# Kernel optimization log

Measured on AMD Instinct MI355X. Metric: run time of the kernel, lower is better.

## Reference

```python
import jax, jax.numpy as jnp
import numpy as np

TAU = 0.05
BETA = 8.0
MAX_ITERS = 6
EPS = 1e-12  # torch F.normalize eps


def setup_inputs() -> dict:
    key = jax.random.key(0)
    P, d, C, h = 20000, 128, 512, 4
    k1, k2, k3, k4 = jax.random.split(key, 4)
    K = jax.random.normal(k1, (P, d), dtype=jnp.float32) * 0.1
    Theta = jax.random.normal(k2, (C, d, h), dtype=jnp.float32)
    head_idx = jax.random.randint(k3, (C,), 0, P)
    initial_val = jax.random.uniform(k4, (P,), dtype=jnp.float32)
    return {"K": K, "Theta": Theta, "head_idx": head_idx, "initial_val": initial_val}


def _l2norm(x, axis):
    n = jnp.sqrt(jnp.sum(x * x, axis=axis, keepdims=True))
    return x / jnp.maximum(n, EPS)


def reference(K, Theta, head_idx, initial_val):
    P = K.shape[0]
    C, d, h = Theta.shape
    Kn = _l2norm(K, axis=1)            # [P, d]
    Thetan = _l2norm(Theta, axis=1)    # [C, d, h] (normalize over d, per slot)
    # cosine similarity per clause/slot: S[c, p, s]
    S = jnp.einsum('pd,cds->cps', Kn, Thetan)          # [C, P, h]
    best = jnp.argmax(S, axis=1)                        # [C, h] best predicate per slot
    conf = jnp.take_along_axis(S, best[:, None, :], axis=1)[:, 0, :]  # [C, h]
    beta_eff = max(BETA, 1.0)
    n = 2 * h
    log_n = jnp.float32(np.log(n))

    val = initial_val
    for _ in range(MAX_ITERS):
        vals = val[best]                                # [C, h] truth values at argmax preds
        combined = jnp.concatenate([conf, vals], axis=1)  # [C, 2h]
        # softmin_tau(x) = -(1/tau) * (logsumexp(-x/tau) - log n)
        g = -(1.0 / TAU) * (jax.nn.logsumexp(-combined / TAU, axis=1) - log_n)
        g = jnp.clip(g, 0.0, 1.0)                       # [C]
        # soft OR per head: (1/beta) * logsumexp(beta * g) over clauses sharing a head
        e = jax.ops.segment_sum(jnp.exp(beta_eff * g), head_idx, num_segments=P)
        g_head = jnp.log(jnp.maximum(e, 1e-38)) / beta_eff
        val = jnp.where(e > 0, jnp.maximum(val, g_head), val)
    return val
```

## Files before the change

### kernel.cpp

```cpp
#include <hip/hip_runtime.h>
#include <hip/hip_bf16.h>
#include <math.h>

#define D_DIM 128
#define H_DIM 4
#define QCAP 1024

typedef __attribute__((ext_vector_type(4))) float f32x4;
typedef __attribute__((ext_vector_type(8))) __bf16 bf16x8v;

__device__ inline unsigned int f2bf(float f) {
    __hip_bfloat16 b = __float2bfloat16(f);
    return (unsigned int)*reinterpret_cast<unsigned short*>(&b);
}
__device__ inline unsigned int encf(float v) {
    unsigned int u = __float_as_uint(v);
    return (u & 0x80000000u) ? ~u : (u | 0x80000000u);
}
__device__ inline float decf(unsigned int ub) {
    unsigned int fb = (ub & 0x80000000u) ? (ub ^ 0x80000000u) : ~ub;
    return __uint_as_float(fb);
}

__global__ __launch_bounds__(256) void k_prep(
    const float* __restrict__ K, unsigned int* __restrict__ Knb,
    float* __restrict__ rnK,
    const float* __restrict__ Theta, unsigned int* __restrict__ Tnb,
    float* __restrict__ Tn32,
    const float* __restrict__ initial, float* __restrict__ out,
    int* __restrict__ head_of, int P, int Ppad, int NJ)
{
    int wave = threadIdx.x >> 6, lane = threadIdx.x & 63;
    int row = blockIdx.x * 4 + wave;
    if (row < Ppad) {
        if (row >= P) {
            Knb[(size_t)row * 64 + lane] = 0u;
        } else {
            float2 v = ((const float2*)(K + (size_t)row * D_DIM))[lane];
            float ss = v.x * v.x + v.y * v.y;
            #pragma unroll
            for (int off = 1; off < 64; off <<= 1) ss += __shfl_xor(ss, off);
            float rn = 1.0f / fmaxf(sqrtf(ss), 1e-12f);
            Knb[(size_t)row * 64 + lane] = f2bf(v.x * rn) | (f2bf(v.y * rn) << 16);
            if (lane == 0) {
                rnK[row] = rn;
                out[row] = initial[row];
                head_of[row] = 0x7FFFFFFF;
            }
        }
    }
    if (blockIdx.x < (NJ >> 2)) {
        int j = blockIdx.x * 4 + wave;
        int c = j >> 2, s = j & 3;
        const float* base = Theta + (size_t)c * (D_DIM * H_DIM) + s;
        float t0 = base[(2 * lane) * H_DIM];
        float t1 = base[(2 * lane + 1) * H_DIM];
        float ss = t0 * t0 + t1 * t1;
        #pragma unroll
        for (int off = 1; off < 64; off <<= 1) ss += __shfl_xor(ss, off);
        float rn = 1.0f / fmaxf(sqrtf(ss), 1e-12f);
        float n0 = t0 * rn, n1 = t1 * rn;
        Tnb[(size_t)j * 64 + lane] = f2bf(n0) | (f2bf(n1) << 16);
        float2 w2; w2.x = n0; w2.y = n1;
        ((float2*)(Tn32 + (size_t)j * D_DIM))[lane] = w2;
    }
}

__global__ __launch_bounds__(256) void k_fused3(
    const unsigned short* __restrict__ Knb, const unsigned short* __restrict__ Tnb,
    const float* __restrict__ K, const float* __restrict__ rnK,
    const float* __restrict__ Tn32,
    unsigned int* __restrict__ gmax, unsigned long long* __restrict__ cand,
    int P)
{
    __shared__ __align__(16) unsigned short As[128 * 128];
    __shared__ __align__(16) unsigned short Bs[128 * 128];
    __shared__ float sred[5 * 512];
    __shared__ float thrl[128];
    __shared__ unsigned short queue[QCAP];
    __shared__ int qn;

    const int tid = threadIdx.x;
    const int lane = tid & 63;
    const int wave = tid >> 6;
    if (tid == 0) qn = 0;

    const int jt = blockIdx.x >> 5;
    const int w  = blockIdx.x & 31;
    const int begin = (w < 29) ? w * 5 : 29 * 5 + (w - 29) * 4;
    const int cnt   = (w < 29) ? 5 : 4;
    const int j0 = jt * 128;

    const int rr = lane >> 4, cc = lane & 15;

    {
        const unsigned short* gA = Tnb + (size_t)j0 * 128;
        const unsigned short* gB = Knb + (size_t)(begin * 128) * 128;
        #pragma unroll
        for (int i = 0; i < 8; i++) {
            int r0 = wave * 32 + i * 4;
            int rw = r0 + rr;
            int sc = (cc ^ (rw & 7)) << 3;
            __builtin_amdgcn_global_load_lds(
                (const __attribute__((address_space(1))) unsigned int*)(gA + (size_t)rw * 128 + sc),
                (__attribute__((address_space(3))) unsigned int*)&As[r0 * 128], 16, 0, 0);
            __builtin_amdgcn_global_load_lds(
                (const __attribute__((address_space(1))) unsigned int*)(gB + (size_t)rw * 128 + sc),
                (__attribute__((address_space(3))) unsigned int*)&Bs[r0 * 128], 16, 0, 0);
        }
    }
    __syncthreads();

    const int wm = wave >> 1, wn = wave & 1;
    const int lr = lane & 15, lg = lane >> 4;
    float runmax = -INFINITY;

    for (int t = 0; t < cnt; t++) {
        f32x4 acc[4][4];
        #pragma unroll
        for (int m = 0; m < 4; m++)
            #pragma unroll
            for (int n = 0; n < 4; n++) { f32x4 z = {0.f, 0.f, 0.f, 0.f}; acc[m][n] = z; }
        #pragma unroll
        for (int ks = 0; ks < 4; ks++) {
            int koff = (8 * lg + 32 * ks) ^ ((lr & 7) << 3);
            bf16x8v af[4], bv[4];
            #pragma unroll
            for (int m = 0; m < 4; m++)
                af[m] = *(const bf16x8v*)&As[(64 * wm + 16 * m + lr) * 128 + koff];
            #pragma unroll
            for (int n = 0; n < 4; n++)
                bv[n] = *(const bf16x8v*)&Bs[(64 * wn + 16 * n + lr) * 128 + koff];
            #pragma unroll
            for (int m = 0; m < 4; m++)
                #pragma unroll
                for (int n = 0; n < 4; n++)
                    acc[m][n] = __builtin_amdgcn_mfma_f32_16x16x32_bf16(af[m], bv[n], acc[m][n], 0, 0, 0);
        }
        __syncthreads();

        if (t + 1 < cnt) {
            const unsigned short* gB = Knb + (size_t)((begin + t + 1) * 128) * 128;
            #pragma unroll
            for (int i = 0; i < 8; i++) {
                int r0 = wave * 32 + i * 4;
                int rw = r0 + rr;
                int sc = (cc ^ (rw & 7)) << 3;
                __builtin_amdgcn_global_load_lds(
                    (const __attribute__((address_space(1))) unsigned int*)(gB + (size_t)rw * 128 + sc),
                    (__attribute__((address_space(3))) unsigned int*)&Bs[r0 * 128], 16, 0, 0);
            }
        }

        #pragma unroll
        for (int m = 0; m < 4; m++) {
            #pragma unroll
            for (int n2 = 0; n2 < 2; n2++) {
                f32x4 a0 = acc[m][2 * n2], a1 = acc[m][2 * n2 + 1];
                float t0 = fmaxf(a0[0], a1[0]);
                float t1 = fmaxf(a0[1], a1[1]);
                float t2 = fmaxf(a0[2], a1[2]);
                float t3 = fmaxf(a0[3], a1[3]);
                #pragma unroll
                for (int off = 1; off <= 8; off <<= 1) {
                    t0 = fmaxf(t0, __shfl_xor(t0, off));
                    t1 = fmaxf(t1, __shfl_xor(t1, off));
                    t2 = fmaxf(t2, __shfl_xor(t2, off));
                    t3 = fmaxf(t3, __shfl_xor(t3, off));
                }
                if (lr == 0) {
                    int jb = 64 * wm + 16 * m + 4 * lg;
                    int ch = 2 * wn + n2;
                    sred[t * 512 + (jb + 0) * 4 + ch] = t0;
                    sred[t * 512 + (jb + 1) * 4 + ch] = t1;
                    sred[t * 512 + (jb + 2) * 4 + ch] = t2;
                    sred[t * 512 + (jb + 3) * 4 + ch] = t3;
                }
            }
        }
        __syncthreads();

        if (tid < 128) {
            const float* sr = &sred[t * 512 + tid * 4];
            float tmax = fmaxf(fmaxf(sr[0], sr[1]), fmaxf(sr[2], sr[3]));
            if (tmax > runmax) {
                runmax = tmax;
                atomicMax(&gmax[j0 + tid], encf(tmax));
            }
        }
    }

    if (tid < 128) {
        unsigned int gv = __hip_atomic_load(&gmax[j0 + tid], __ATOMIC_RELAXED,
                                            __HIP_MEMORY_SCOPE_AGENT);
        thrl[tid] = decf(gv) - 0.009f;
    }
    __syncthreads();

    for (int e = tid; e < cnt * 512; e += 256) {
        int jl = (e >> 2) & 127;
        if (sred[e] >= thrl[jl]) {
            int qi = atomicAdd(&qn, 1);
            if (qi < QCAP) queue[qi] = (unsigned short)e;
        }
    }
    __syncthreads();

    int nq = qn;
    bool ovf = (nq > QCAP);
    int tot = ovf ? cnt * 512 : nq;
    int half = lane & 1, pl = lane >> 1;
    for (int i = wave; i < tot; i += 4) {
        int e = ovf ? i : (int)queue[i];
        int t = e >> 9, rem = e & 511;
        int jl = rem >> 2, ch = rem & 3;
        int j = j0 + jl;
        int p = (begin + t) * 128 + ch * 32 + pl;
        bool ok = (p < P);
        int pc = ok ? p : 0;
        const float4* kp = (const float4*)(K + (size_t)pc * D_DIM + half * 64);
        const float4* tp = (const float4*)(Tn32 + (size_t)j * D_DIM + half * 64);
        float sx = 0.f, sy = 0.f, sz = 0.f, sw = 0.f;
        #pragma unroll
        for (int k4 = 0; k4 < 16; k4++) {
            float4 a = kp[k4], bb = tp[k4];
            sx = fmaf(a.x, bb.x, sx); sy = fmaf(a.y, bb.y, sy);
            sz = fmaf(a.z, bb.z, sz); sw = fmaf(a.w, bb.w, sw);
        }
        float dot = (sx + sy) + (sz + sw);
        dot += __shfl_xor(dot, 1);
        float v = ok ? dot * rnK[pc] : -INFINITY;
        int bp = p;
        #pragma unroll
        for (int off = 2; off < 64; off <<= 1) {
            float ov = __shfl_xor(v, off);
            int op = __shfl_xor(bp, off);
            if (ov > v || (ov == v && op < bp)) { v = ov; bp = op; }
        }
        if (lane == 0) {
            unsigned long long key =
                ((unsigned long long)encf(v) << 32) | (unsigned int)(0x7FFFFFFF - bp);
            atomicMax(&cand[j], key);
        }
    }
}

__global__ __launch_bounds__(512) void k_logic2(
    const int* __restrict__ head_idx, const float* __restrict__ initial_val,
    const unsigned long long* __restrict__ cand, int* __restrict__ head_of,
    float* __restrict__ out, int C)
{
    __shared__ float hval[512];
    __shared__ float elds[512];
    int c = threadIdx.x;
    int h = head_idx[c];
    atomicMin(&head_of[h], c);
    __syncthreads();
    int myslot = __hip_atomic_load(&head_of[h], __ATOMIC_RELAXED, __HIP_MEMORY_SCOPE_AGENT);
    hval[c] = initial_val[h];

    float cf[H_DIM], v0[H_DIM]; int bs[H_DIM];
    #pragma unroll
    for (int s = 0; s < H_DIM; s++) {
        unsigned long long key = cand[c * H_DIM + s];
        cf[s] = decf((unsigned int)(key >> 32));
        int b = 0x7FFFFFFF - (int)(key & 0xFFFFFFFFu);
        v0[s] = initial_val[b];
        int ho = __hip_atomic_load(&head_of[b], __ATOMIC_RELAXED, __HIP_MEMORY_SCOPE_AGENT);
        bs[s] = (ho < C) ? ho : -1;
    }
    __syncthreads();

    const float inv_tau = 20.0f;
    const float logn = logf(2.0f * H_DIM);
    const float beta = 8.0f;

    for (int it = 0; it < 6; it++) {
        float x[2 * H_DIM];
        #pragma unroll
        for (int s = 0; s < H_DIM; s++) {
            x[s] = cf[s];
            x[H_DIM + s] = (bs[s] >= 0) ? hval[bs[s]] : v0[s];
        }
        float cur = hval[myslot];
        elds[c] = 0.f;
        __syncthreads();

        float m = x[0];
        #pragma unroll
        for (int i = 1; i < 2 * H_DIM; i++) m = fminf(m, x[i]);
        float ssum = 0.f;
        #pragma unroll
        for (int i = 0; i < 2 * H_DIM; i++) ssum += expf((m - x[i]) * inv_tau);
        float g = -inv_tau * ((-m * inv_tau + logf(ssum)) - logn);
        g = fminf(fmaxf(g, 0.f), 1.f);
        atomicAdd(&elds[myslot], expf(beta * g));
        __syncthreads();

        float e = elds[myslot];
        float gh = logf(fmaxf(e, 1e-38f)) / beta;
        float nv = fmaxf(cur, gh);
        if (myslot == c) hval[c] = nv;
        __syncthreads();
    }

    if (myslot == c) out[h] = hval[c];
}

extern "C" void kernel_launch(void* const* d_in, const int* in_sizes, int n_in,
                              void* d_out, int out_size, void* d_ws, size_t ws_size,
                              hipStream_t stream) {
    const float* K        = (const float*)d_in[0];
    const float* Theta    = (const float*)d_in[1];
    const int*   head_idx = (const int*)d_in[2];
    const float* initial  = (const float*)d_in[3];
    float* out = (float*)d_out;

    int P  = in_sizes[3];
    int C  = in_sizes[2];
    int NJ = C * H_DIM;
    int Ppad = ((P + 127) / 128) * 128;
    (void)ws_size; (void)n_in; (void)out_size;

    char* w = (char*)d_ws;
    size_t off = 0;
    auto alloc = [&](size_t bytes) { void* p = w + off; off += (bytes + 255) & ~(size_t)255; return p; };
    unsigned int* Knb  = (unsigned int*)alloc((size_t)Ppad * D_DIM * 2);
    unsigned int* Tnb  = (unsigned int*)alloc((size_t)NJ * D_DIM * 2);
    float* Tn32 = (float*)alloc((size_t)NJ * D_DIM * 4);
    float* rnK  = (float*)alloc((size_t)P * 4);
    unsigned int* gmax       = (unsigned int*)alloc((size_t)NJ * 4);
    unsigned long long* cand = (unsigned long long*)alloc((size_t)NJ * 8);
    int* head_of             = (int*)alloc((size_t)P * 4);

    k_prep<<<Ppad / 4, 256, 0, stream>>>(K, Knb, rnK, Theta, Tnb, Tn32,
                                         initial, out, head_of, P, Ppad, NJ);
    k_fused3<<<512, 256, 0, stream>>>((const unsigned short*)Knb,
                                      (const unsigned short*)Tnb,
                                      K, rnK, Tn32, gmax, cand, P);
    k_logic2<<<1, C, 0, stream>>>(head_idx, initial, cand, head_of, out, C);
}
```

Measured before the change: 75.12 us.

## Use 512-thread blocks with 8 waves and move per-tile maxima to global scratch

Doubles the fused GEMM/argmax kernel to 8 waves per block, each covering a 64x32 sub-tile, so each wave holds fewer accumulators and more waves can hide latency. The per-tile partial maxima move from shared memory to a per-block global scratch buffer to free LDS. Each wave now issues its own atomicMax per row, which drops one block barrier and the separate reduction pass. The cost is more global atomics and global-memory traffic for the candidate scan, which reads the scratch back after a block barrier.

```diff
diff --git a/kernel.cpp b/kernel.cpp
--- a/kernel.cpp
+++ b/kernel.cpp
@@ -66,16 +66,15 @@
     }
 }
 
-__global__ __launch_bounds__(256) void k_fused3(
+__global__ __launch_bounds__(512, 4) void k_fused4(
     const unsigned short* __restrict__ Knb, const unsigned short* __restrict__ Tnb,
     const float* __restrict__ K, const float* __restrict__ rnK,
-    const float* __restrict__ Tn32,
+    const float* __restrict__ Tn32, float* __restrict__ sredG,
     unsigned int* __restrict__ gmax, unsigned long long* __restrict__ cand,
     int P)
 {
     __shared__ __align__(16) unsigned short As[128 * 128];
     __shared__ __align__(16) unsigned short Bs[128 * 128];
-    __shared__ float sred[5 * 512];
     __shared__ float thrl[128];
     __shared__ unsigned short queue[QCAP];
     __shared__ int qn;
@@ -90,6 +89,7 @@
     const int begin = (w < 29) ? w * 5 : 29 * 5 + (w - 29) * 4;
     const int cnt   = (w < 29) ? 5 : 4;
     const int j0 = jt * 128;
+    float* myred = sredG + (size_t)blockIdx.x * (5 * 512);
 
     const int rr = lane >> 4, cc = lane & 15;
 
@@ -97,8 +97,8 @@
         const unsigned short* gA = Tnb + (size_t)j0 * 128;
         const unsigned short* gB = Knb + (size_t)(begin * 128) * 128;
         #pragma unroll
-        for (int i = 0; i < 8; i++) {
-            int r0 = wave * 32 + i * 4;
+        for (int i = 0; i < 4; i++) {
+            int r0 = wave * 16 + i * 4;
             int rw = r0 + rr;
             int sc = (cc ^ (rw & 7)) << 3;
             __builtin_amdgcn_global_load_lds(
@@ -109,32 +109,37 @@
                 (__attribute__((address_space(3))) unsigned int*)&Bs[r0 * 128], 16, 0, 0);
         }
     }
-    __syncthreads();
-
-    const int wm = wave >> 1, wn = wave & 1;
+
+    const int wm = wave >> 2, wn = wave & 3;
     const int lr = lane & 15, lg = lane >> 4;
-    float runmax = -INFINITY;
+    float rm[4][4];
+    #pragma unroll
+    for (int m = 0; m < 4; m++)
+        #pragma unroll
+        for (int r = 0; r < 4; r++) rm[m][r] = -INFINITY;
 
     for (int t = 0; t < cnt; t++) {
-        f32x4 acc[4][4];
+        __syncthreads();
+
+        f32x4 acc[4][2];
         #pragma unroll
         for (int m = 0; m < 4; m++)
             #pragma unroll
-            for (int n = 0; n < 4; n++) { f32x4 z = {0.f, 0.f, 0.f, 0.f}; acc[m][n] = z; }
+            for (int n = 0; n < 2; n++) { f32x4 z = {0.f, 0.f, 0.f, 0.f}; acc[m][n] = z; }
         #pragma unroll
         for (int ks = 0; ks < 4; ks++) {
             int koff = (8 * lg + 32 * ks) ^ ((lr & 7) << 3);
-            bf16x8v af[4], bv[4];
+            bf16x8v af[4], bv[2];
             #pragma unroll
             for (int m = 0; m < 4; m++)
                 af[m] = *(const bf16x8v*)&As[(64 * wm + 16 * m + lr) * 128 + koff];
             #pragma unroll
-            for (int n = 0; n < 4; n++)
-                bv[n] = *(const bf16x8v*)&Bs[(64 * wn + 16 * n + lr) * 128 + koff];
+            for (int n = 0; n < 2; n++)
+                bv[n] = *(const bf16x8v*)&Bs[(32 * wn + 16 * n + lr) * 128 + koff];
             #pragma unroll
             for (int m = 0; m < 4; m++)
                 #pragma unroll
-                for (int n = 0; n < 4; n++)
+                for (int n = 0; n < 2; n++)
                     acc[m][n] = __builtin_amdgcn_mfma_f32_16x16x32_bf16(af[m], bv[n], acc[m][n], 0, 0, 0);
         }
         __syncthreads();
@@ -142,8 +147,8 @@
         if (t + 1 < cnt) {
             const unsigned short* gB = Knb + (size_t)((begin + t + 1) * 128) * 128;
             #pragma unroll
-            for (int i = 0; i < 8; i++) {
-                int r0 = wave * 32 + i * 4;
+            for (int i = 0; i < 4; i++) {
+                int r0 = wave * 16 + i * 4;
                 int rw = r0 + rr;
                 int sc = (cc ^ (rw & 7)) << 3;
                 __builtin_amdgcn_global_load_lds(
@@ -154,38 +159,29 @@
 
         #pragma unroll
         for (int m = 0; m < 4; m++) {
-            #pragma unroll
-            for (int n2 = 0; n2 < 2; n2++) {
-                f32x4 a0 = acc[m][2 * n2], a1 = acc[m][2 * n2 + 1];
-                float t0 = fmaxf(a0[0], a1[0]);
-                float t1 = fmaxf(a0[1], a1[1]);
-                float t2 = fmaxf(a0[2], a1[2]);
-                float t3 = fmaxf(a0[3], a1[3]);
+            f32x4 a0 = acc[m][0], a1 = acc[m][1];
+            float t0 = fmaxf(a0[0], a1[0]);
+            float t1 = fmaxf(a0[1], a1[1]);
+            float t2 = fmaxf(a0[2], a1[2]);
+            float t3 = fmaxf(a0[3], a1[3]);
+            #pragma unroll
+            for (int off = 1; off <= 8; off <<= 1) {
+                t0 = fmaxf(t0, __shfl_xor(t0, off));
+                t1 = fmaxf(t1, __shfl_xor(t1, off));
+                t2 = fmaxf(t2, __shfl_xor(t2, off));
+                t3 = fmaxf(t3, __shfl_xor(t3, off));
+            }
+            if (lr == 0) {
+                int jb = 64 * wm + 16 * m + 4 * lg;
+                float tv[4] = { t0, t1, t2, t3 };
                 #pragma unroll
-                for (int off = 1; off <= 8; off <<= 1) {
-                    t0 = fmaxf(t0, __shfl_xor(t0, off));
-                    t1 = fmaxf(t1, __shfl_xor(t1, off));
-                    t2 = fmaxf(t2, __shfl_xor(t2, off));
-                    t3 = fmaxf(t3, __shfl_xor(t3, off));
+                for (int r = 0; r < 4; r++) {
+                    myred[t * 512 + (jb + r) * 4 + wn] = tv[r];
+                    if (tv[r] > rm[m][r]) {
+                        rm[m][r] = tv[r];
+                        atomicMax(&gmax[j0 + jb + r], encf(tv[r]));
+                    }
                 }
-                if (lr == 0) {
-                    int jb = 64 * wm + 16 * m + 4 * lg;
-                    int ch = 2 * wn + n2;
-                    sred[t * 512 + (jb + 0) * 4 + ch] = t0;
-                    sred[t * 512 + (jb + 1) * 4 + ch] = t1;
-                    sred[t * 512 + (jb + 2) * 4 + ch] = t2;
-                    sred[t * 512 + (jb + 3) * 4 + ch] = t3;
-                }
-            }
-        }
-        __syncthreads();
-
-        if (tid < 128) {
-            const float* sr = &sred[t * 512 + tid * 4];
-            float tmax = fmaxf(fmaxf(sr[0], sr[1]), fmaxf(sr[2], sr[3]));
-            if (tmax > runmax) {
-                runmax = tmax;
-                atomicMax(&gmax[j0 + tid], encf(tmax));
             }
         }
     }
@@ -197,9 +193,9 @@
     }
     __syncthreads();
 
-    for (int e = tid; e < cnt * 512; e += 256) {
+    for (int e = tid; e < cnt * 512; e += 512) {
         int jl = (e >> 2) & 127;
-        if (sred[e] >= thrl[jl]) {
+        if (myred[e] >= thrl[jl]) {
             int qi = atomicAdd(&qn, 1);
             if (qi < QCAP) queue[qi] = (unsigned short)e;
         }
@@ -210,7 +206,7 @@
     bool ovf = (nq > QCAP);
     int tot = ovf ? cnt * 512 : nq;
     int half = lane & 1, pl = lane >> 1;
-    for (int i = wave; i < tot; i += 4) {
+    for (int i = wave; i < tot; i += 8) {
         int e = ovf ? i : (int)queue[i];
         int t = e >> 9, rem = e & 511;
         int jl = rem >> 2, ch = rem & 3;
@@ -329,14 +325,15 @@
     unsigned int* Tnb  = (unsigned int*)alloc((size_t)NJ * D_DIM * 2);
     float* Tn32 = (float*)alloc((size_t)NJ * D_DIM * 4);
     float* rnK  = (float*)alloc((size_t)P * 4);
+    float* sredG = (float*)alloc((size_t)512 * 5 * 512 * 4);
     unsigned int* gmax       = (unsigned int*)alloc((size_t)NJ * 4);
     unsigned long long* cand = (unsigned long long*)alloc((size_t)NJ * 8);
     int* head_of             = (int*)alloc((size_t)P * 4);
 
     k_prep<<<Ppad / 4, 256, 0, stream>>>(K, Knb, rnK, Theta, Tnb, Tn32,
                                          initial, out, head_of, P, Ppad, NJ);
-    k_fused3<<<512, 256, 0, stream>>>((const unsigned short*)Knb,
+    k_fused4<<<512, 512, 0, stream>>>((const unsigned short*)Knb,
                                       (const unsigned short*)Tnb,
-                                      K, rnK, Tn32, gmax, cand, P);
+                                      K, rnK, Tn32, sredG, gmax, cand, P);
     k_logic2<<<1, C, 0, stream>>>(head_idx, initial, cand, head_of, out, C);
 }
```

New measurement: 99.79 us. 1.33x slower.

## Stream K tiles directly from global into registers, widen grid to 768 blocks

Applied to the files above, without the earlier changes.

Removes the LDS staging buffer for the K operand. Each wave now loads its B fragments straight from global memory into registers, which drops the per-tile barriers and frees LDS so more blocks can be resident. The grid grows from 32 to 48 column splits per row tile, giving 3-4 tiles per block instead of 4-5. Per-tile maxima go to global memory through atomicMax from each writer lane, guarded by a relaxed load, and the same load-then-atomic guard is added to the candidate atomics. The trade-off is uncoalesced direct global loads of K through cache and more atomic traffic in exchange for occupancy and fewer synchronisations.

```diff
diff --git a/kernel.cpp b/kernel.cpp
--- a/kernel.cpp
+++ b/kernel.cpp
@@ -66,7 +66,7 @@
     }
 }
 
-__global__ __launch_bounds__(256) void k_fused3(
+__global__ __launch_bounds__(256) void k_fused7(
     const unsigned short* __restrict__ Knb, const unsigned short* __restrict__ Tnb,
     const float* __restrict__ K, const float* __restrict__ rnK,
     const float* __restrict__ Tn32,
@@ -74,8 +74,7 @@
     int P)
 {
     __shared__ __align__(16) unsigned short As[128 * 128];
-    __shared__ __align__(16) unsigned short Bs[128 * 128];
-    __shared__ float sred[5 * 512];
+    __shared__ float sred[4 * 512];
     __shared__ float thrl[128];
     __shared__ unsigned short queue[QCAP];
     __shared__ int qn;
@@ -85,17 +84,15 @@
     const int wave = tid >> 6;
     if (tid == 0) qn = 0;
 
-    const int jt = blockIdx.x >> 5;
-    const int w  = blockIdx.x & 31;
-    const int begin = (w < 29) ? w * 5 : 29 * 5 + (w - 29) * 4;
-    const int cnt   = (w < 29) ? 5 : 4;
+    const int jt = blockIdx.x / 48;
+    const int w  = blockIdx.x % 48;
+    const int begin = (w < 13) ? w * 4 : 13 * 4 + (w - 13) * 3;
+    const int cnt   = (w < 13) ? 4 : 3;
     const int j0 = jt * 128;
 
-    const int rr = lane >> 4, cc = lane & 15;
-
     {
+        int rr = lane >> 4, cc = lane & 15;
         const unsigned short* gA = Tnb + (size_t)j0 * 128;
-        const unsigned short* gB = Knb + (size_t)(begin * 128) * 128;
         #pragma unroll
         for (int i = 0; i < 8; i++) {
             int r0 = wave * 32 + i * 4;
@@ -104,52 +101,39 @@
             __builtin_amdgcn_global_load_lds(
                 (const __attribute__((address_space(1))) unsigned int*)(gA + (size_t)rw * 128 + sc),
                 (__attribute__((address_space(3))) unsigned int*)&As[r0 * 128], 16, 0, 0);
-            __builtin_amdgcn_global_load_lds(
-                (const __attribute__((address_space(1))) unsigned int*)(gB + (size_t)rw * 128 + sc),
-                (__attribute__((address_space(3))) unsigned int*)&Bs[r0 * 128], 16, 0, 0);
         }
     }
     __syncthreads();
 
     const int wm = wave >> 1, wn = wave & 1;
     const int lr = lane & 15, lg = lane >> 4;
-    float runmax = -INFINITY;
 
     for (int t = 0; t < cnt; t++) {
+        const int p0 = (begin + t) * 128;
+        const unsigned short* gB = Knb + (size_t)p0 * 128 + 8 * lg;
+
         f32x4 acc[4][4];
         #pragma unroll
         for (int m = 0; m < 4; m++)
             #pragma unroll
             for (int n = 0; n < 4; n++) { f32x4 z = {0.f, 0.f, 0.f, 0.f}; acc[m][n] = z; }
+
         #pragma unroll
         for (int ks = 0; ks < 4; ks++) {
+            bf16x8v bv[4];
+            #pragma unroll
+            for (int n = 0; n < 4; n++)
+                bv[n] = *(const bf16x8v*)&gB[(size_t)(64 * wn + 16 * n + lr) * 128 + 32 * ks];
             int koff = (8 * lg + 32 * ks) ^ ((lr & 7) << 3);
-            bf16x8v af[4], bv[4];
+            bf16x8v af[4];
             #pragma unroll
             for (int m = 0; m < 4; m++)
                 af[m] = *(const bf16x8v*)&As[(64 * wm + 16 * m + lr) * 128 + koff];
-            #pragma unroll
-            for (int n = 0; n < 4; n++)
-                bv[n] = *(const bf16x8v*)&Bs[(64 * wn + 16 * n + lr) * 128 + koff];
             #pragma unroll
             for (int m = 0; m < 4; m++)
                 #pragma unroll
                 for (int n = 0; n < 4; n++)
                     acc[m][n] = __builtin_amdgcn_mfma_f32_16x16x32_bf16(af[m], bv[n], acc[m][n], 0, 0, 0);
-        }
-        __syncthreads();
-
-        if (t + 1 < cnt) {
-            const unsigned short* gB = Knb + (size_t)((begin + t + 1) * 128) * 128;
-            #pragma unroll
-            for (int i = 0; i < 8; i++) {
-                int r0 = wave * 32 + i * 4;
-                int rw = r0 + rr;
-                int sc = (cc ^ (rw & 7)) << 3;
-                __builtin_amdgcn_global_load_lds(
-                    (const __attribute__((address_space(1))) unsigned int*)(gB + (size_t)rw * 128 + sc),
-                    (__attribute__((address_space(3))) unsigned int*)&Bs[r0 * 128], 16, 0, 0);
-            }
         }
 
         #pragma unroll
@@ -171,24 +155,21 @@
                 if (lr == 0) {
                     int jb = 64 * wm + 16 * m + 4 * lg;
                     int ch = 2 * wn + n2;
-                    sred[t * 512 + (jb + 0) * 4 + ch] = t0;
-                    sred[t * 512 + (jb + 1) * 4 + ch] = t1;
-                    sred[t * 512 + (jb + 2) * 4 + ch] = t2;
-                    sred[t * 512 + (jb + 3) * 4 + ch] = t3;
+                    float tv[4] = { t0, t1, t2, t3 };
+                    #pragma unroll
+                    for (int r = 0; r < 4; r++) {
+                        sred[t * 512 + (jb + r) * 4 + ch] = tv[r];
+                        unsigned int ev = encf(tv[r]);
+                        unsigned int cur = __hip_atomic_load(&gmax[j0 + jb + r],
+                                                             __ATOMIC_RELAXED,
+                                                             __HIP_MEMORY_SCOPE_AGENT);
+                        if (ev > cur) atomicMax(&gmax[j0 + jb + r], ev);
+                    }
                 }
             }
         }
-        __syncthreads();
-
-        if (tid < 128) {
-            const float* sr = &sred[t * 512 + tid * 4];
-            float tmax = fmaxf(fmaxf(sr[0], sr[1]), fmaxf(sr[2], sr[3]));
-            if (tmax > runmax) {
-                runmax = tmax;
-                atomicMax(&gmax[j0 + tid], encf(tmax));
-            }
-        }
-    }
+    }
+    __syncthreads();
 
     if (tid < 128) {
         unsigned int gv = __hip_atomic_load(&gmax[j0 + tid], __ATOMIC_RELAXED,
@@ -240,7 +221,9 @@
         if (lane == 0) {
             unsigned long long key =
                 ((unsigned long long)encf(v) << 32) | (unsigned int)(0x7FFFFFFF - bp);
-            atomicMax(&cand[j], key);
+            unsigned long long curk = __hip_atomic_load(&cand[j], __ATOMIC_RELAXED,
+                                                        __HIP_MEMORY_SCOPE_AGENT);
+            if (key > curk) atomicMax(&cand[j], key);
         }
     }
 }
@@ -335,8 +318,8 @@
 
     k_prep<<<Ppad / 4, 256, 0, stream>>>(K, Knb, rnK, Theta, Tnb, Tn32,
                                          initial, out, head_of, P, Ppad, NJ);
-    k_fused3<<<512, 256, 0, stream>>>((const unsigned short*)Knb,
-                                      (const unsigned short*)Tnb,
-                                      K, rnK, Tn32, gmax, cand, P);
+    k_fused7<<<16 * 48, 256, 0, stream>>>((const unsigned short*)Knb,
+                                          (const unsigned short*)Tnb,
+                                          K, rnK, Tn32, gmax, cand, P);
     k_logic2<<<1, C, 0, stream>>>(head_idx, initial, cand, head_of, out, C);
 }
```

After: 111.3 us. 1.48x slower.
